# Kernel optimization log

Measured on AMD Instinct MI355X. Metric: run time of the kernel, lower is better.

## Reference

```python
import jax, jax.numpy as jnp
import numpy as np

B, DIM, N_SIDE = 32, 256, 32
HEADS, DIM_K, DIM_U = 4, 16, 1
DIM_V = 64  # dim_out // heads
EPS = 1e-5

def _rel_pos_idx(n):
    # matches calc_rel_pos: meshgrid(ij) -> (N,2), pairwise diff + (n-1)
    i = np.arange(n)
    pos = np.stack(np.meshgrid(i, i, indexing='ij'), 0).reshape(2, -1).T  # (N, 2)
    rel = pos[None, :] - pos[:, None] + (n - 1)                            # (N, N, 2)
    return rel[..., 0], rel[..., 1]

def _bn(t, gamma, beta):
    # BatchNorm2d in training mode: batch stats over (B, H, W), biased var
    mu = t.mean(axis=(0, 2, 3), keepdims=True)
    var = t.var(axis=(0, 2, 3), keepdims=True)
    xhat = (t - mu) * jax.lax.rsqrt(var + EPS)
    return xhat * gamma[None, :, None, None] + beta[None, :, None, None]

def setup_inputs() -> dict:
    key = jax.random.key(0)
    ks = jax.random.split(key, 5)
    rl = 2 * N_SIDE - 1
    return {
        'x': jax.random.normal(ks[0], (B, DIM, N_SIDE, N_SIDE), jnp.float32),
        'w_q': jax.random.normal(ks[1], (DIM_K * HEADS, DIM), jnp.float32) * 0.05,
        'w_k': jax.random.normal(ks[2], (DIM_K * DIM_U, DIM), jnp.float32) * 0.05,
        'w_v': jax.random.normal(ks[3], (DIM_V * DIM_U, DIM), jnp.float32) * 0.05,
        'gamma_q': jnp.ones((DIM_K * HEADS,), jnp.float32),
        'beta_q': jnp.zeros((DIM_K * HEADS,), jnp.float32),
        'gamma_v': jnp.ones((DIM_V * DIM_U,), jnp.float32),
        'beta_v': jnp.zeros((DIM_V * DIM_U,), jnp.float32),
        'rel_pos_emb': jax.random.normal(ks[4], (rl, rl, DIM_K, DIM_U), jnp.float32),
    }

def reference(x, w_q, w_k, w_v, gamma_q, beta_q, gamma_v, beta_v, rel_pos_emb):
    b, c, hh, ww = x.shape
    n = hh * ww
    # 1x1 convs as channel contractions
    q = _bn(jnp.einsum('oc,bchw->bohw', w_q, x), gamma_q, beta_q)
    k = jnp.einsum('oc,bchw->bohw', w_k, x)
    v = _bn(jnp.einsum('oc,bchw->bohw', w_v, x), gamma_v, beta_v)
    q = q.reshape(b, HEADS, DIM_K, n)   # b h k n
    k = k.reshape(b, DIM_U, DIM_K, n)   # b u k m
    v = v.reshape(b, DIM_U, DIM_V, n)   # b u v m
    k = jax.nn.softmax(k, axis=-1)
    # content lambda
    lam_c = jnp.einsum('bukm,buvm->bkv', k, v)
    Yc = jnp.einsum('bhkn,bkv->bhvn', q, lam_c)
    # positional lambda via relative-position embedding gather
    ni, mi = _rel_pos_idx(N_SIDE)
    emb = rel_pos_emb[ni, mi]                      # (n, n, k, u)
    lam_p = jnp.einsum('nmku,buvm->bnkv', emb, v)  # dominant compute
    Yp = jnp.einsum('bhkn,bnkv->bhvn', q, lam_p)
    Y = Yc + Yp                                    # b h v n
    return Y.reshape(b, HEADS * DIM_V, hh, ww)
```

## Files before the change

### kernel.cpp

```cpp
#include <hip/hip_runtime.h>

using u16 = unsigned short;
using u32 = unsigned int;

typedef __attribute__((ext_vector_type(4))) float f32x4;
typedef __attribute__((ext_vector_type(4))) u16 u16x4;
typedef __attribute__((ext_vector_type(8))) u16 u16x8;
typedef __attribute__((ext_vector_type(8))) short s16x8;

__device__ __forceinline__ u16 f2bf(float f) {
  u32 x = __builtin_bit_cast(u32, f);
  x += 0x7fffu + ((x >> 16) & 1u);
  return (u16)(x >> 16);
}
__device__ __forceinline__ float bf2f(u16 u) {
  u32 x = ((u32)u) << 16;
  return __builtin_bit_cast(float, x);
}

__device__ __forceinline__ void glds16(const u16* gsrc, u16* ldst) {
  __builtin_amdgcn_global_load_lds(
      (const __attribute__((address_space(1))) unsigned int*)gsrc,
      (__attribute__((address_space(3))) unsigned int*)ldst, 16, 0, 0);
}

__global__ __launch_bounds__(256) void k_prep(
    const float* __restrict__ wq, const float* __restrict__ wk,
    const float* __restrict__ wv, const float* __restrict__ R,
    u16* __restrict__ Wb, u16* __restrict__ APre, float* __restrict__ zbuf)
{
  const int blk = blockIdx.x;
  const int t = threadIdx.x;
  if (blk < 129) zbuf[blk * 256 + t] = 0.f;
  if (blk < 144) {
    const int o = blk;
    const float* src = (o < 64) ? (wq + o * 256)
                     : (o < 80) ? (wk + (o - 64) * 256)
                                : (wv + (o - 80) * 256);
    Wb[o * 256 + t] = f2bf(src[t]);
  } else {
    const int di = blk - 144;
    const int w = t >> 6, l = t & 63;
    const int g = l >> 4, k = l & 15;
    for (int j1 = w; j1 < 32; j1 += 4) {
      u16x8 o8;
#pragma unroll
      for (int e = 0; e < 8; ++e) {
        int dj = 8 * g + e - j1 + 31;
        o8[e] = f2bf(R[(di * 63 + dj) * 16 + k]);
      }
      *(u16x8*)(APre + ((di * 32 + j1) * 64 + l) * 8) = o8;
    }
  }
}

union ProjSmem {
  u16 XLb[64][264];
  float SS[2][160];
};

__global__ __launch_bounds__(256) void k_proj(
    const float* __restrict__ x, const u16* __restrict__ Wb,
    float* __restrict__ q_raw, float* __restrict__ k_raw,
    float* __restrict__ v_raw,
    float* __restrict__ qs1, float* __restrict__ qs2,
    float* __restrict__ vs1, float* __restrict__ vs2)
{
  __shared__ ProjSmem PS;
  const int b  = blockIdx.x >> 4;
  const int p0 = (blockIdx.x & 15) * 64;
  const int t  = threadIdx.x;

  {
    const int p4 = (t & 15) * 4;
    const int cb = (t >> 4);
#pragma unroll
    for (int i = 0; i < 8; ++i) {
      const int c = 2 * (i * 16 + cb);
      f32x4 xa = *(const f32x4*)&x[(b * 256 + c) * 1024 + p0 + p4];
      f32x4 xb = *(const f32x4*)&x[(b * 256 + c + 1) * 1024 + p0 + p4];
#pragma unroll
      for (int j = 0; j < 4; ++j) {
        u32 pk = (u32)f2bf(xa[j]) | ((u32)f2bf(xb[j]) << 16);
        *(u32*)&PS.XLb[p4 + j][c] = pk;
      }
    }
  }
  __syncthreads();

  const int w  = t >> 6;
  const int l  = t & 63;
  const int g  = l >> 4;
  const int cc = l & 15;
  const int p  = p0 + w * 16 + cc;

  f32x4 acc[9];
  const f32x4 fz = {0.f, 0.f, 0.f, 0.f};
#pragma unroll
  for (int mt = 0; mt < 9; ++mt) acc[mt] = fz;

#pragma unroll
  for (int ko = 0; ko < 8; ++ko) {
    s16x8 bfr = *(const s16x8*)&PS.XLb[w * 16 + cc][ko * 32 + g * 8];
#pragma unroll
    for (int mt = 0; mt < 9; ++mt) {
      s16x8 afr = *(const s16x8*)&Wb[(mt * 16 + cc) * 256 + ko * 32 + g * 8];
      acc[mt] = __builtin_amdgcn_mfma_f32_16x16x32_bf16(afr, bfr, acc[mt], 0, 0, 0);
    }
  }

#pragma unroll
  for (int mt = 0; mt < 9; ++mt) {
#pragma unroll
    for (int r = 0; r < 4; ++r) {
      const int o = mt * 16 + 4 * g + r;
      const float val = acc[mt][r];
      if (mt < 4)       q_raw[(b * 64 + o) * 1024 + p] = val;
      else if (mt == 4) k_raw[(b * 16 + (o - 64)) * 1024 + p] = val;
      else              v_raw[(b * 64 + (o - 80)) * 1024 + p] = val;
    }
  }

  __syncthreads();
  {
    float* ss = &PS.SS[0][0];
    for (int i = t; i < 320; i += 256) ss[i] = 0.f;
  }
  __syncthreads();
#pragma unroll
  for (int mt = 0; mt < 9; ++mt) {
    if (mt == 4) continue;
#pragma unroll
    for (int r = 0; r < 4; ++r) {
      float s1 = acc[mt][r];
      float s2 = s1 * s1;
#pragma unroll
      for (int off = 1; off < 16; off <<= 1) {
        s1 += __shfl_xor(s1, off);
        s2 += __shfl_xor(s2, off);
      }
      if (cc == 0) {
        const int o = mt * 16 + 4 * g + r;
        atomicAdd(&PS.SS[0][o], s1);
        atomicAdd(&PS.SS[1][o], s2);
      }
    }
  }
  __syncthreads();
  if (t < 64) {
    atomicAdd(&qs1[t], PS.SS[0][t]);
    atomicAdd(&qs2[t], PS.SS[1][t]);
  } else if (t >= 80 && t < 144) {
    atomicAdd(&vs1[t - 80], PS.SS[0][t]);
    atomicAdd(&vs2[t - 80], PS.SS[1][t]);
  }
}

__global__ __launch_bounds__(256) void k_nl(
    const float* __restrict__ v_raw,
    const float* __restrict__ vs1, const float* __restrict__ vs2,
    const float* __restrict__ gv, const float* __restrict__ bv,
    const float* __restrict__ k_raw,
    u16* __restrict__ vnF, float* __restrict__ lam_c)
{
  __shared__ float VN[64][136];
  __shared__ float KE[16][132];
  __shared__ float KMX[16], KIV[16];
  const int b  = blockIdx.x >> 3;
  const int m0 = (blockIdx.x & 7) * 128;
  const int t  = threadIdx.x;
  const int wv4 = t >> 6, lane = t & 63;

  for (int rr = wv4; rr < 16; rr += 4) {
    const int row = b * 16 + rr;
    const f32x4* kr4 = (const f32x4*)(k_raw + row * 1024 + lane * 16);
    f32x4 a0 = kr4[0], a1 = kr4[1], a2 = kr4[2], a3 = kr4[3];
    float mx = -3.0e38f;
#pragma unroll
    for (int j = 0; j < 4; ++j)
      mx = fmaxf(mx, fmaxf(fmaxf(a0[j], a1[j]), fmaxf(a2[j], a3[j])));
#pragma unroll
    for (int off = 32; off; off >>= 1) mx = fmaxf(mx, __shfl_xor(mx, off));
    float s = 0.f;
#pragma unroll
    for (int j = 0; j < 4; ++j)
      s += __expf(a0[j] - mx) + __expf(a1[j] - mx)
         + __expf(a2[j] - mx) + __expf(a3[j] - mx);
#pragma unroll
    for (int off = 32; off; off >>= 1) s += __shfl_xor(s, off);
    if (lane == 0) { KMX[rr] = mx; KIV[rr] = 1.0f / s; }
  }

  {
    const int v = t & 63, mseg = t >> 6;
    const float invN = 1.0f / 32768.0f;
    const float mu = vs1[v] * invN;
    const float var = vs2[v] * invN - mu * mu;
    const float sc = rsqrtf(var + 1e-5f) * gv[v];
    const float bi = bv[v] - mu * sc;
    const int i2 = (m0 >> 5) + mseg;
    const float* src = v_raw + (b * 64 + v) * 1024 + i2 * 32;
    u16* dstF = vnF + ((b * 32 + i2) * 4 + (v >> 4)) * 512 + (v & 15) * 8;
#pragma unroll
    for (int lg = 0; lg < 4; ++lg) {
      f32x4 a = *(const f32x4*)(src + lg * 8);
      f32x4 c = *(const f32x4*)(src + lg * 8 + 4);
      f32x4 na, nc;
      u16x8 o8;
#pragma unroll
      for (int j = 0; j < 4; ++j) {
        na[j] = a[j] * sc + bi;
        nc[j] = c[j] * sc + bi;
        o8[j] = f2bf(na[j]);
        o8[4 + j] = f2bf(nc[j]);
      }
      *(f32x4*)&VN[v][mseg * 32 + lg * 8] = na;
      *(f32x4*)&VN[v][mseg * 32 + lg * 8 + 4] = nc;
      *(u16x8*)(dstF + lg * 128) = o8;
    }
  }
  __syncthreads();

  {
    const int kc = t >> 4, mm = (t & 15) * 8;
    const float* kr = k_raw + (b * 16 + kc) * 1024 + m0 + mm;
    const float mx = KMX[kc], iv = KIV[kc];
#pragma unroll
    for (int j = 0; j < 8; ++j) KE[kc][mm + j] = __expf(kr[j] - mx) * iv;
  }
  __syncthreads();

  const int kc = t & 15, vg = t >> 4;
  float acc[4] = {0.f, 0.f, 0.f, 0.f};
  for (int m4 = 0; m4 < 128; m4 += 4) {
    f32x4 ke = *(const f32x4*)&KE[kc][m4];
#pragma unroll
    for (int j = 0; j < 4; ++j) {
      f32x4 vv = *(const f32x4*)&VN[vg * 4 + j][m4];
      acc[j] += ke[0] * vv[0] + ke[1] * vv[1] + ke[2] * vv[2] + ke[3] * vv[3];
    }
  }
#pragma unroll
  for (int j = 0; j < 4; ++j)
    atomicAdd(&lam_c[(b * 16 + kc) * 64 + vg * 4 + j], acc[j]);
}

__device__ __forceinline__ void load_a4(s16x8 (&dst)[4], const u16* ab)
{
#pragma unroll
  for (int j = 0; j < 4; ++j) dst[j] = *(const s16x8*)(ab + j * 512);
}

union KMainSmem {
  u16 BB[2][8192];
  float YL[256][18];
};

__global__ __launch_bounds__(256, 4) void k_main(
    const u16* __restrict__ APre, const u16* __restrict__ vnF,
    const float* __restrict__ q_raw, const float* __restrict__ lam_c,
    const float* __restrict__ qs1, const float* __restrict__ qs2,
    const float* __restrict__ gq, const float* __restrict__ bq,
    float* __restrict__ out)
{
  __shared__ alignas(16) KMainSmem S;
  __shared__ float QL[64][17];
  const int bid  = blockIdx.x;
  const int xcd  = bid & 7;
  const int sb   = bid >> 3;
  const int b    = xcd * 4 + (sb & 3);
  const int rest = sb >> 2;
  const int i1   = rest >> 1;
  const int half = rest & 1;
  const int t  = threadIdx.x;
  const int w  = t >> 6;
  const int l  = t & 63;
  const int g  = l >> 4;
  const int c  = l & 15;
  const int j1base = half * 16 + w * 4;

  const u16* vF = vnF + b * 65536;

  f32x4 acc[4][4];
  const f32x4 fz = {0.f, 0.f, 0.f, 0.f};
#pragma unroll
  for (int nn = 0; nn < 4; ++nn)
#pragma unroll
    for (int tt = 0; tt < 4; ++tt) acc[nn][tt] = fz;

  {
    const int o = t >> 2, ns = (t & 3) * 4;
    const float invN = 1.0f / 32768.0f;
    const float mu = qs1[o] * invN;
    const float var = qs2[o] * invN - mu * mu;
    const float rs = rsqrtf(var + 1e-5f);
    const float sc = rs * gq[o];
    const float bi = bq[o] - mu * sc;
    f32x4 qa = *(const f32x4*)&q_raw[(b * 64 + o) * 1024 + i1 * 32 + half * 16 + ns];
#pragma unroll
    for (int j = 0; j < 4; ++j) QL[o][ns + j] = qa[j] * sc + bi;
  }
  {
    const u16* src = vF + w * 2048 + l * 8;
    u16* dst = &S.BB[0][w * 2048];
#pragma unroll
    for (int j = 0; j < 4; ++j) glds16(src + j * 512, dst + j * 512);
  }

  s16x8 afrP[4], afrQ[4];
  const u16* aBase = APre + ((31 - i1) * 32 + j1base) * 512 + l * 8;
  load_a4(afrP, aBase);
  __syncthreads();

  for (int p = 0; p < 8; ++p) {
    const int cur = p & 1;
    const bool pf = (p < 7);
    if (pf) {
      const u16* src = vF + (p + 1) * 8192 + w * 2048 + l * 8;
      u16* dst = &S.BB[cur ^ 1][w * 2048];
#pragma unroll
      for (int j = 0; j < 4; ++j) glds16(src + j * 512, dst + j * 512);
    }
    __builtin_amdgcn_sched_barrier(0);
    const u16* ap = aBase + 4 * p * 16384;
    s16x8 bfr[4];
#pragma unroll
    for (int s = 0; s < 4; ++s) {
#pragma unroll
      for (int tt = 0; tt < 4; ++tt)
        bfr[tt] = *(const s16x8*)&S.BB[cur][s * 2048 + tt * 512 + l * 8];
      if (s < 3) {
        if (s & 1) load_a4(afrP, ap + (s + 1) * 16384);
        else       load_a4(afrQ, ap + (s + 1) * 16384);
      } else if (pf) {
        load_a4(afrP, ap + 4 * 16384);
      }
      const s16x8* A = (s & 1) ? afrQ : afrP;
#pragma unroll
      for (int nn = 0; nn < 4; ++nn)
#pragma unroll
        for (int tt = 0; tt < 4; ++tt)
          acc[nn][tt] = __builtin_amdgcn_mfma_f32_16x16x32_bf16(
              A[nn], bfr[tt], acc[nn][tt], 0, 0, 0);
    }
    asm volatile("s_waitcnt vmcnt(4)" ::: "memory");
    __builtin_amdgcn_sched_barrier(0);
    __builtin_amdgcn_s_barrier();
    __builtin_amdgcn_sched_barrier(0);
  }

  {
    const float* lcb = lam_c + b * 1024;
#pragma unroll
    for (int tt = 0; tt < 4; ++tt)
#pragma unroll
      for (int r = 0; r < 4; ++r) {
        const float lv = lcb[(4 * g + r) * 64 + tt * 16 + c];
#pragma unroll
        for (int nn = 0; nn < 4; ++nn) acc[nn][tt][r] += lv;
      }
  }
#pragma unroll
  for (int nn = 0; nn < 4; ++nn) {
    const int j1loc = w * 4 + nn;
#pragma unroll
    for (int h = 0; h < 4; ++h) {
      const float q0 = QL[h * 16 + 4 * g + 0][j1loc];
      const float q1 = QL[h * 16 + 4 * g + 1][j1loc];
      const float q2 = QL[h * 16 + 4 * g + 2][j1loc];
      const float q3 = QL[h * 16 + 4 * g + 3][j1loc];
#pragma unroll
      for (int tt = 0; tt < 4; ++tt) {
        float sY = q0 * acc[nn][tt][0] + q1 * acc[nn][tt][1]
                 + q2 * acc[nn][tt][2] + q3 * acc[nn][tt][3];
        sY += __shfl_xor(sY, 16);
        sY += __shfl_xor(sY, 32);
        if (g == h) S.YL[h * 64 + tt * 16 + c][j1loc] = sY;
      }
    }
  }
  __syncthreads();
#pragma unroll
  for (int it = 0; it < 4; ++it) {
    const int o  = (t >> 2) + it * 64;
    const int nf = (t & 3) * 4;
    f32x4 v4 = *(const f32x4*)&S.YL[o][nf];
    *(f32x4*)&out[(b * 256 + o) * 1024 + i1 * 32 + half * 16 + nf] = v4;
  }
}

extern "C" void kernel_launch(void* const* d_in, const int* in_sizes, int n_in,
                              void* d_out, int out_size, void* d_ws, size_t ws_size,
                              hipStream_t stream) {
  const float* x  = (const float*)d_in[0];
  const float* wq = (const float*)d_in[1];
  const float* wk = (const float*)d_in[2];
  const float* wv = (const float*)d_in[3];
  const float* gq = (const float*)d_in[4];
  const float* bq = (const float*)d_in[5];
  const float* gv = (const float*)d_in[6];
  const float* bv = (const float*)d_in[7];
  const float* R  = (const float*)d_in[8];
  float* out = (float*)d_out;

  float* wsf   = (float*)d_ws;
  float* q_raw = wsf;
  float* k_raw = q_raw + 32 * 64 * 1024;
  float* v_raw = k_raw + 32 * 16 * 1024;
  float* lam_c = v_raw + 32 * 64 * 1024;
  float* qs1   = lam_c + 32 * 16 * 64;
  float* qs2   = qs1 + 64;
  float* vs1   = qs2 + 64;
  float* vs2   = vs1 + 64;
  float* kmax  = vs2 + 64;
  float* kinv  = kmax + 512;
  u16*   vn    = (u16*)(kinv + 512);
  u16*   vnF   = vn + 32 * 64 * 1024;
  u16*   APre  = vnF + 32 * 65536;
  u16*   Wb    = APre + 63 * 32 * 512;

  k_prep<<<207, 256, 0, stream>>>(wq, wk, wv, R, Wb, APre, lam_c);
  k_proj<<<512, 256, 0, stream>>>(x, Wb, q_raw, k_raw, v_raw, qs1, qs2, vs1, vs2);
  k_nl<<<256, 256, 0, stream>>>(v_raw, vs1, vs2, gv, bv, k_raw, vnF, lam_c);
  k_main<<<2048, 256, 0, stream>>>(APre, vnF, q_raw, lam_c, qs1, qs2, gq, bq, out);
}
```

Baseline: 134.4 us.

## Switch main GEMM from 16x16x32 to 32x32x16 bf16 MFMA with re-laid operands

Replaces the 16 small 16x16x32 MFMAs per k-step with 8 larger 32x32x16 MFMAs. To feed them, the precomputed positional embedding layout (APre) and the normalized V fragment layout (vnF) are rearranged, and the epilogue that adds lam_c and contracts with q is rewritten for the 32x32 accumulator register mapping. The larger MFMA issues fewer instructions for the same work and may run at higher throughput, but the index remapping is error-prone and the epilogue reduction changes shape.

```diff
diff --git a/kernel.cpp b/kernel.cpp
--- a/kernel.cpp
+++ b/kernel.cpp
@@ -4,6 +4,7 @@
 using u32 = unsigned int;
 
 typedef __attribute__((ext_vector_type(4))) float f32x4;
+typedef __attribute__((ext_vector_type(16))) float f32x16;
 typedef __attribute__((ext_vector_type(4))) u16 u16x4;
 typedef __attribute__((ext_vector_type(8))) u16 u16x8;
 typedef __attribute__((ext_vector_type(8))) short s16x8;
@@ -41,15 +42,17 @@
   } else {
     const int di = blk - 144;
     const int w = t >> 6, l = t & 63;
-    const int g = l >> 4, k = l & 15;
-    for (int j1 = w; j1 < 32; j1 += 4) {
+    const int jp = (l >> 4) & 1, k = l & 15, kb = (l >> 5) * 8;
+    for (int idx = w; idx < 32; idx += 4) {
+      const int j1p = idx >> 1, j2h = idx & 1;
+      const int j1 = 2 * j1p + jp;
       u16x8 o8;
 #pragma unroll
       for (int e = 0; e < 8; ++e) {
-        int dj = 8 * g + e - j1 + 31;
+        const int dj = j2h * 16 + kb + e - j1 + 31;
         o8[e] = f2bf(R[(di * 63 + dj) * 16 + k]);
       }
-      *(u16x8*)(APre + ((di * 32 + j1) * 64 + l) * 8) = o8;
+      *(u16x8*)(APre + ((di * 16 + j1p) * 2 + j2h) * 512 + l * 8) = o8;
     }
   }
 }
@@ -200,7 +203,8 @@
     const float bi = bv[v] - mu * sc;
     const int i2 = (m0 >> 5) + mseg;
     const float* src = v_raw + (b * 64 + v) * 1024 + i2 * 32;
-    u16* dstF = vnF + ((b * 32 + i2) * 4 + (v >> 4)) * 512 + (v & 15) * 8;
+    const int vh = v >> 5, vl = v & 31;
+    u16* dstB = vnF + ((b * 32 + i2) * 4) * 512;
 #pragma unroll
     for (int lg = 0; lg < 4; ++lg) {
       f32x4 a = *(const f32x4*)(src + lg * 8);
@@ -216,7 +220,7 @@
       }
       *(f32x4*)&VN[v][mseg * 32 + lg * 8] = na;
       *(f32x4*)&VN[v][mseg * 32 + lg * 8 + 4] = nc;
-      *(u16x8*)(dstF + lg * 128) = o8;
+      *(u16x8*)(dstB + ((lg >> 1) * 2 + vh) * 512 + (vl + 32 * (lg & 1)) * 8) = o8;
     }
   }
   __syncthreads();
@@ -275,18 +279,18 @@
   const int t  = threadIdx.x;
   const int w  = t >> 6;
   const int l  = t & 63;
-  const int g  = l >> 4;
-  const int c  = l & 15;
-  const int j1base = half * 16 + w * 4;
+  const int lh = l >> 5;
+  const int j1pbase = half * 8 + w * 2;
 
   const u16* vF = vnF + b * 65536;
 
-  f32x4 acc[4][4];
-  const f32x4 fz = {0.f, 0.f, 0.f, 0.f};
-#pragma unroll
-  for (int nn = 0; nn < 4; ++nn)
-#pragma unroll
-    for (int tt = 0; tt < 4; ++tt) acc[nn][tt] = fz;
+  f32x16 acc[2][2];
+#pragma unroll
+  for (int mt = 0; mt < 2; ++mt)
+#pragma unroll
+    for (int vg = 0; vg < 2; ++vg)
+#pragma unroll
+      for (int r = 0; r < 16; ++r) acc[mt][vg][r] = 0.f;
 
   {
     const int o = t >> 2, ns = (t & 3) * 4;
@@ -308,7 +312,7 @@
   }
 
   s16x8 afrP[4], afrQ[4];
-  const u16* aBase = APre + ((31 - i1) * 32 + j1base) * 512 + l * 8;
+  const u16* aBase = APre + ((31 - i1) * 16 + j1pbase) * 1024 + l * 8;
   load_a4(afrP, aBase);
   __syncthreads();
 
@@ -327,8 +331,8 @@
 #pragma unroll
     for (int s = 0; s < 4; ++s) {
 #pragma unroll
-      for (int tt = 0; tt < 4; ++tt)
-        bfr[tt] = *(const s16x8*)&S.BB[cur][s * 2048 + tt * 512 + l * 8];
+      for (int f = 0; f < 4; ++f)
+        bfr[f] = *(const s16x8*)&S.BB[cur][s * 2048 + f * 512 + l * 8];
       if (s < 3) {
         if (s & 1) load_a4(afrP, ap + (s + 1) * 16384);
         else       load_a4(afrQ, ap + (s + 1) * 16384);
@@ -336,12 +340,14 @@
         load_a4(afrP, ap + 4 * 16384);
       }
       const s16x8* A = (s & 1) ? afrQ : afrP;
-#pragma unroll
-      for (int nn = 0; nn < 4; ++nn)
-#pragma unroll
-        for (int tt = 0; tt < 4; ++tt)
-          acc[nn][tt] = __builtin_amdgcn_mfma_f32_16x16x32_bf16(
-              A[nn], bfr[tt], acc[nn][tt], 0, 0, 0);
+      acc[0][0] = __builtin_amdgcn_mfma_f32_32x32x16_bf16(A[0], bfr[0], acc[0][0], 0, 0, 0);
+      acc[0][1] = __builtin_amdgcn_mfma_f32_32x32x16_bf16(A[0], bfr[1], acc[0][1], 0, 0, 0);
+      acc[1][0] = __builtin_amdgcn_mfma_f32_32x32x16_bf16(A[2], bfr[0], acc[1][0], 0, 0, 0);
+      acc[1][1] = __builtin_amdgcn_mfma_f32_32x32x16_bf16(A[2], bfr[1], acc[1][1], 0, 0, 0);
+      acc[0][0] = __builtin_amdgcn_mfma_f32_32x32x16_bf16(A[1], bfr[2], acc[0][0], 0, 0, 0);
+      acc[0][1] = __builtin_amdgcn_mfma_f32_32x32x16_bf16(A[1], bfr[3], acc[0][1], 0, 0, 0);
+      acc[1][0] = __builtin_amdgcn_mfma_f32_32x32x16_bf16(A[3], bfr[2], acc[1][0], 0, 0, 0);
+      acc[1][1] = __builtin_amdgcn_mfma_f32_32x32x16_bf16(A[3], bfr[3], acc[1][1], 0, 0, 0);
     }
     asm volatile("s_waitcnt vmcnt(4)" ::: "memory");
     __builtin_amdgcn_sched_barrier(0);
@@ -352,30 +358,38 @@
   {
     const float* lcb = lam_c + b * 1024;
 #pragma unroll
-    for (int tt = 0; tt < 4; ++tt)
-#pragma unroll
-      for (int r = 0; r < 4; ++r) {
-        const float lv = lcb[(4 * g + r) * 64 + tt * 16 + c];
-#pragma unroll
-        for (int nn = 0; nn < 4; ++nn) acc[nn][tt][r] += lv;
-      }
-  }
-#pragma unroll
-  for (int nn = 0; nn < 4; ++nn) {
-    const int j1loc = w * 4 + nn;
-#pragma unroll
-    for (int h = 0; h < 4; ++h) {
-      const float q0 = QL[h * 16 + 4 * g + 0][j1loc];
-      const float q1 = QL[h * 16 + 4 * g + 1][j1loc];
-      const float q2 = QL[h * 16 + 4 * g + 2][j1loc];
-      const float q3 = QL[h * 16 + 4 * g + 3][j1loc];
-#pragma unroll
-      for (int tt = 0; tt < 4; ++tt) {
-        float sY = q0 * acc[nn][tt][0] + q1 * acc[nn][tt][1]
-                 + q2 * acc[nn][tt][2] + q3 * acc[nn][tt][3];
-        sY += __shfl_xor(sY, 16);
-        sY += __shfl_xor(sY, 32);
-        if (g == h) S.YL[h * 64 + tt * 16 + c][j1loc] = sY;
+    for (int vg = 0; vg < 2; ++vg)
+#pragma unroll
+      for (int reg = 0; reg < 16; ++reg) {
+        const int k = (reg & 3) + 8 * ((reg >> 2) & 1) + 4 * lh;
+        const float lv = lcb[k * 64 + vg * 32 + (l & 31)];
+        acc[0][vg][reg] += lv;
+        acc[1][vg][reg] += lv;
+      }
+  }
+#pragma unroll
+  for (int mt = 0; mt < 2; ++mt) {
+#pragma unroll
+    for (int jp = 0; jp < 2; ++jp) {
+      const int j1loc = 2 * (w * 2 + mt) + jp;
+#pragma unroll
+      for (int h = 0; h < 4; ++h) {
+        float qv[8];
+#pragma unroll
+        for (int rr = 0; rr < 8; ++rr) {
+          const int k = (rr & 3) + 8 * ((rr >> 2) & 1) + 4 * lh;
+          qv[rr] = QL[h * 16 + k][j1loc];
+        }
+#pragma unroll
+        for (int vg = 0; vg < 2; ++vg) {
+          float sY = 0.f;
+#pragma unroll
+          for (int rr = 0; rr < 8; ++rr)
+            sY += qv[rr] * acc[mt][vg][jp * 8 + rr];
+          sY += __shfl_xor(sY, 32);
+          if ((h >> 1) == lh)
+            S.YL[h * 64 + vg * 32 + (l & 31)][j1loc] = sY;
+        }
       }
     }
   }
@@ -418,7 +432,6 @@
   u16*   vnF   = vn + 32 * 64 * 1024;
   u16*   APre  = vnF + 32 * 65536;
   u16*   Wb    = APre + 63 * 32 * 512;
-
   k_prep<<<207, 256, 0, stream>>>(wq, wk, wv, R, Wb, APre, lam_c);
   k_proj<<<512, 256, 0, stream>>>(x, Wb, q_raw, k_raw, v_raw, qs1, qs2, vs1, vs2);
   k_nl<<<256, 256, 0, stream>>>(v_raw, vs1, vs2, gv, bv, k_raw, vnF, lam_c);
```

Measured after the change: 135.6 us. Within noise of the previous version (+0.9%).
